# Performance work log

Measured on AMD Instinct MI355X. Metric: run time of the kernel, lower is better.

## Reference

```python
import jax, jax.numpy as jnp
import numpy as np

DECAY = 0.9
BETA_OBS = 1.0
BETA_STATE = 1.0

N_OBS = 20000
N_STATES = 1024
N_ACTIONS = 64
STATE_DIM = 256
RFD = 2048


def setup_inputs() -> dict:
    key = jax.random.key(0)
    ks = jax.random.split(key, 7)
    Q = jax.random.normal(ks[0], (STATE_DIM, N_STATES), dtype=jnp.float32) / np.sqrt(STATE_DIM).astype(np.float32)
    V = jax.random.normal(ks[1], (STATE_DIM, N_ACTIONS), dtype=jnp.float32) / np.sqrt(STATE_DIM).astype(np.float32)
    W = jax.random.normal(ks[2], (RFD, STATE_DIM), dtype=jnp.float32)
    M_re = jax.random.normal(ks[3], (RFD, N_OBS), dtype=jnp.float32)
    M_im = jax.random.normal(ks[4], (RFD, N_OBS), dtype=jnp.float32)
    obs = jax.random.uniform(ks[5], (N_OBS,), dtype=jnp.float32)
    action = jax.random.uniform(ks[6], (N_ACTIONS,), dtype=jnp.float32)
    return {"Q": Q, "V": V, "W": W, "M_re": M_re, "M_im": M_im, "obs": obs, "action": action}


def reference(Q, V, W, M_re, M_im, obs, action):
    # One fused POCML step: memory write (decayed outer product), state
    # rotation via complex random-feature phase, clean_up (state-kernel
    # softmax retrieval), and obs retrieval from memory.
    D = W.shape[0]  # random_feature_dim
    M = M_re + 1j * M_im                       # [D, n_obs] complex64
    obs_c = obs.astype(jnp.complex64)
    # get_state_from_memory
    state0 = M @ obs_c                         # [D]
    # update_memory: M *= decay; M += outer(state, obs)
    M_new = DECAY * M + jnp.outer(state0, obs_c)
    # update_state: v = V @ action; phi_v = exp(1j * W @ v); state *= phi_v
    v = V @ action                             # [state_dim]
    phi_v = jnp.exp(1j * (W @ v))              # [D] complex64
    state1 = state0 * phi_v
    # clean_up: phi_Q = exp(1j * W @ Q), weights = softmax(beta*sim(phi_Q.T, state))
    phi_Q = jnp.exp(1j * (W @ Q))              # [D, n_states]
    score = BETA_STATE * (phi_Q.T @ jnp.conj(state1)).real / D  # [n_states]
    weights = jax.nn.softmax(score)
    state2 = phi_Q @ weights.astype(jnp.complex64)              # [D]
    # get_obs_from_memory: softmax(beta_obs * sim(M.T, state))
    obs_score = BETA_OBS * (M_new.T @ jnp.conj(state2)).real / D  # [n_obs]
    return jax.nn.softmax(obs_score)
```

## Files before the change

### kernel.cpp

```cpp
#include <hip/hip_runtime.h>
#include <math.h>

#define N_OBS    20000
#define N_OBS4   5000
#define N_STATES 1024
#define N_ACT    64
#define SDIM     256
#define RFD      2048
#define DECAY    0.9f

#define OFF_S0RE   0
#define OFF_S0IM   2048
#define OFF_S1RE   4096
#define OFF_S1IM   6144
#define OFF_S2RE   8192
#define OFF_S2IM   10240
#define OFF_SCORE  12288
#define OFF_DOT0   13312
#define OFF_OBSACC 13316
#define OFF_WTS    33316
#define OFF_COSQ   34816
#define OFF_SINQ   (34816 + RFD*N_STATES)
#define WS_FLOATS  (OFF_SINQ + RFD*N_STATES)
#define ZERO_OFF   OFF_SCORE
#define ZERO_CNT   (OFF_OBSACC + N_OBS - OFF_SCORE)

__global__ __launch_bounds__(256) void k_state0(
    const float* __restrict__ Mre, const float* __restrict__ Mim,
    const float* __restrict__ obs, float* __restrict__ s0re, float* __restrict__ s0im)
{
    __shared__ float r1[256], r2[256];
    const int d = blockIdx.x, tid = threadIdx.x;
    const float4* mr = (const float4*)(Mre + (size_t)d * N_OBS);
    const float4* mi = (const float4*)(Mim + (size_t)d * N_OBS);
    const float4* ob = (const float4*)obs;
    float ar = 0.f, ai = 0.f;
    for (int idx = tid; idx < N_OBS4; idx += 256) {
        float4 o = ob[idx];
        float4 a = mr[idx];
        float4 b = mi[idx];
        ar += a.x*o.x + a.y*o.y + a.z*o.z + a.w*o.w;
        ai += b.x*o.x + b.y*o.y + b.z*o.z + b.w*o.w;
    }
    r1[tid] = ar; r2[tid] = ai; __syncthreads();
    for (int s = 128; s > 0; s >>= 1) {
        if (tid < s) { r1[tid] += r1[tid+s]; r2[tid] += r2[tid+s]; }
        __syncthreads();
    }
    if (tid == 0) { s0re[d] = r1[0]; s0im[d] = r2[0]; }
}

__global__ __launch_bounds__(256) void k_state1(
    const float* __restrict__ V, const float* __restrict__ action,
    const float* __restrict__ W,
    const float* __restrict__ s0re, const float* __restrict__ s0im,
    float* __restrict__ s1re, float* __restrict__ s1im)
{
    __shared__ float vsh[SDIM];
    const int tid = threadIdx.x;
    float acc = 0.f;
    for (int a = 0; a < N_ACT; a++) acc += V[tid * N_ACT + a] * action[a];
    vsh[tid] = acc;
    __syncthreads();
    const int d = blockIdx.x * 256 + tid;
    const float* wr = W + (size_t)d * SDIM;
    float th = 0.f;
    #pragma unroll 8
    for (int k = 0; k < SDIM; k++) th += wr[k] * vsh[k];
    float sn, cs;
    sincosf(th, &sn, &cs);
    const float re = s0re[d], im = s0im[d];
    s1re[d] = re * cs - im * sn;
    s1im[d] = re * sn + im * cs;
}

__global__ __launch_bounds__(256) void k_phiQ(
    const float* __restrict__ W, const float* __restrict__ Q,
    const float* __restrict__ s1re, const float* __restrict__ s1im,
    float* __restrict__ cosQ, float* __restrict__ sinQ, float* __restrict__ score)
{
    __shared__ float As[16][65];
    __shared__ float Bs[16][64];
    __shared__ float sscore[64];
    const int tid = threadIdx.x;
    const int tx = tid & 15;
    const int ty = tid >> 4;
    const int m0 = blockIdx.y * 64;
    const int n0 = blockIdx.x * 64;
    float c[4][4] = {};
    for (int k0 = 0; k0 < SDIM; k0 += 16) {
        {
            int k = tid & 15, mb = tid >> 4;
            #pragma unroll
            for (int j = 0; j < 4; j++)
                As[k][mb + 16*j] = W[(size_t)(m0 + mb + 16*j) * SDIM + k0 + k];
        }
        {
            int n = tid & 63, kb = tid >> 6;
            #pragma unroll
            for (int j = 0; j < 4; j++)
                Bs[kb + 4*j][n] = Q[(size_t)(k0 + kb + 4*j) * N_STATES + n0 + n];
        }
        __syncthreads();
        #pragma unroll
        for (int kk = 0; kk < 16; kk++) {
            float a[4], b[4];
            #pragma unroll
            for (int i = 0; i < 4; i++) a[i] = As[kk][ty*4 + i];
            #pragma unroll
            for (int j = 0; j < 4; j++) b[j] = Bs[kk][tx*4 + j];
            #pragma unroll
            for (int i = 0; i < 4; i++)
                #pragma unroll
                for (int j = 0; j < 4; j++)
                    c[i][j] += a[i] * b[j];
        }
        __syncthreads();
    }
    if (tid < 64) sscore[tid] = 0.f;
    __syncthreads();
    float sre[4], sim[4];
    #pragma unroll
    for (int i = 0; i < 4; i++) {
        int d = m0 + ty*4 + i;
        sre[i] = s1re[d]; sim[i] = s1im[d];
    }
    #pragma unroll
    for (int j = 0; j < 4; j++) {
        float pj = 0.f;
        #pragma unroll
        for (int i = 0; i < 4; i++) {
            int d = m0 + ty*4 + i;
            int s = n0 + tx*4 + j;
            float sn, cs;
            sincosf(c[i][j], &sn, &cs);
            cosQ[(size_t)d * N_STATES + s] = cs;
            sinQ[(size_t)d * N_STATES + s] = sn;
            pj += cs * sre[i] + sn * sim[i];
        }
        atomicAdd(&sscore[tx*4 + j], pj);
    }
    __syncthreads();
    if (tid < 64) atomicAdd(&score[n0 + tid], sscore[tid]);
}

__global__ __launch_bounds__(256) void k_softmax_w(
    const float* __restrict__ score, float* __restrict__ wts)
{
    __shared__ float red[256];
    const int tid = threadIdx.x;
    const float scale = 1.f / (float)RFD;
    float4 v = ((const float4*)score)[tid];
    v.x *= scale; v.y *= scale; v.z *= scale; v.w *= scale;
    float mx = fmaxf(fmaxf(v.x, v.y), fmaxf(v.z, v.w));
    red[tid] = mx; __syncthreads();
    for (int s = 128; s > 0; s >>= 1) {
        if (tid < s) red[tid] = fmaxf(red[tid], red[tid+s]);
        __syncthreads();
    }
    mx = red[0]; __syncthreads();
    float4 e;
    e.x = expf(v.x - mx); e.y = expf(v.y - mx);
    e.z = expf(v.z - mx); e.w = expf(v.w - mx);
    red[tid] = e.x + e.y + e.z + e.w; __syncthreads();
    for (int s = 128; s > 0; s >>= 1) {
        if (tid < s) red[tid] += red[tid+s];
        __syncthreads();
    }
    const float inv = 1.f / red[0];
    e.x *= inv; e.y *= inv; e.z *= inv; e.w *= inv;
    ((float4*)wts)[tid] = e;
}

__global__ __launch_bounds__(256) void k_state2(
    const float* __restrict__ cosQ, const float* __restrict__ sinQ,
    const float* __restrict__ wts,
    const float* __restrict__ s0re, const float* __restrict__ s0im,
    float* __restrict__ s2re, float* __restrict__ s2im, float* __restrict__ dot0)
{
    __shared__ float r1[256], r2[256];
    const int d = blockIdx.x, tid = threadIdx.x;
    float4 w = ((const float4*)wts)[tid];
    float4 a = ((const float4*)(cosQ + (size_t)d * N_STATES))[tid];
    float4 b = ((const float4*)(sinQ + (size_t)d * N_STATES))[tid];
    r1[tid] = a.x*w.x + a.y*w.y + a.z*w.z + a.w*w.w;
    r2[tid] = b.x*w.x + b.y*w.y + b.z*w.z + b.w*w.w;
    __syncthreads();
    for (int s = 128; s > 0; s >>= 1) {
        if (tid < s) { r1[tid] += r1[tid+s]; r2[tid] += r2[tid+s]; }
        __syncthreads();
    }
    if (tid == 0) {
        float rc = r1[0], rs = r2[0];
        s2re[d] = rc; s2im[d] = rs;
        atomicAdd(dot0, s0re[d]*rc + s0im[d]*rs);
    }
}

__global__ __launch_bounds__(256) void k_obs_acc(
    const float* __restrict__ Mre, const float* __restrict__ Mim,
    const float* __restrict__ s2re, const float* __restrict__ s2im,
    float* __restrict__ obs_acc)
{
    __shared__ float c_s[64], s_s[64];
    const int tid = threadIdx.x;
    const int dbase = blockIdx.y * 64;
    if (tid < 64) { c_s[tid] = s2re[dbase + tid]; s_s[tid] = s2im[dbase + tid]; }
    __syncthreads();
    const int idx = blockIdx.x * 256 + tid;
    if (idx < N_OBS4) {
        const float4* mr = (const float4*)Mre;
        const float4* mi = (const float4*)Mim;
        float4 acc = make_float4(0.f, 0.f, 0.f, 0.f);
        #pragma unroll 4
        for (int j = 0; j < 64; j++) {
            size_t base = (size_t)(dbase + j) * N_OBS4 + idx;
            float4 a = mr[base];
            float4 b = mi[base];
            float cc = c_s[j], ss = s_s[j];
            acc.x += a.x*cc + b.x*ss;
            acc.y += a.y*cc + b.y*ss;
            acc.z += a.z*cc + b.z*ss;
            acc.w += a.w*cc + b.w*ss;
        }
        atomicAdd(&obs_acc[idx*4 + 0], acc.x);
        atomicAdd(&obs_acc[idx*4 + 1], acc.y);
        atomicAdd(&obs_acc[idx*4 + 2], acc.z);
        atomicAdd(&obs_acc[idx*4 + 3], acc.w);
    }
}

__global__ __launch_bounds__(1024) void k_softmax_obs(
    const float* __restrict__ obs_acc, const float* __restrict__ obs,
    const float* __restrict__ dot0, float* __restrict__ out)
{
    __shared__ float red[1024];
    const int tid = threadIdx.x;
    const float d0 = *dot0;
    const float scale = 1.f / (float)RFD;
    float vals[20];
    float mx = -3.402823466e+38f;
    #pragma unroll
    for (int i = 0; i < 20; i++) {
        int idx = tid + i * 1024;
        if (idx < N_OBS) {
            float sc = (DECAY * obs_acc[idx] + obs[idx] * d0) * scale;
            vals[i] = sc;
            mx = fmaxf(mx, sc);
        } else vals[i] = -3.402823466e+38f;
    }
    red[tid] = mx; __syncthreads();
    for (int s = 512; s > 0; s >>= 1) {
        if (tid < s) red[tid] = fmaxf(red[tid], red[tid+s]);
        __syncthreads();
    }
    mx = red[0]; __syncthreads();
    float sum = 0.f;
    #pragma unroll
    for (int i = 0; i < 20; i++) {
        int idx = tid + i * 1024;
        if (idx < N_OBS) {
            vals[i] = expf(vals[i] - mx);
            sum += vals[i];
        }
    }
    red[tid] = sum; __syncthreads();
    for (int s = 512; s > 0; s >>= 1) {
        if (tid < s) red[tid] += red[tid+s];
        __syncthreads();
    }
    const float inv = 1.f / red[0];
    #pragma unroll
    for (int i = 0; i < 20; i++) {
        int idx = tid + i * 1024;
        if (idx < N_OBS) out[idx] = vals[i] * inv;
    }
}

extern "C" void kernel_launch(void* const* d_in, const int* in_sizes, int n_in,
                              void* d_out, int out_size, void* d_ws, size_t ws_size,
                              hipStream_t stream) {
    const float* Q      = (const float*)d_in[0];
    const float* V      = (const float*)d_in[1];
    const float* W      = (const float*)d_in[2];
    const float* Mre    = (const float*)d_in[3];
    const float* Mim    = (const float*)d_in[4];
    const float* obs    = (const float*)d_in[5];
    const float* action = (const float*)d_in[6];
    float* out = (float*)d_out;
    float* ws  = (float*)d_ws;

    if (ws_size < (size_t)WS_FLOATS * sizeof(float)) return;

    float* s0re  = ws + OFF_S0RE;
    float* s0im  = ws + OFF_S0IM;
    float* s1re  = ws + OFF_S1RE;
    float* s1im  = ws + OFF_S1IM;
    float* s2re  = ws + OFF_S2RE;
    float* s2im  = ws + OFF_S2IM;
    float* score = ws + OFF_SCORE;
    float* dot0  = ws + OFF_DOT0;
    float* oacc  = ws + OFF_OBSACC;
    float* wts   = ws + OFF_WTS;
    float* cosQ  = ws + OFF_COSQ;
    float* sinQ  = ws + OFF_SINQ;

    hipMemsetAsync(ws + ZERO_OFF, 0, (size_t)ZERO_CNT * sizeof(float), stream);

    k_state0<<<RFD, 256, 0, stream>>>(Mre, Mim, obs, s0re, s0im);
    k_state1<<<RFD / 256, 256, 0, stream>>>(V, action, W, s0re, s0im, s1re, s1im);
    k_phiQ<<<dim3(N_STATES / 64, RFD / 64), 256, 0, stream>>>(W, Q, s1re, s1im, cosQ, sinQ, score);
    k_softmax_w<<<1, 256, 0, stream>>>(score, wts);
    k_state2<<<RFD, 256, 0, stream>>>(cosQ, sinQ, wts, s0re, s0im, s2re, s2im, dot0);
    k_obs_acc<<<dim3((N_OBS4 + 255) / 256, RFD / 64), 256, 0, stream>>>(Mre, Mim, s2re, s2im, oacc);
    k_softmax_obs<<<1, 1024, 0, stream>>>(oacc, obs, dot0, out);
}
```

Baseline: 489.0 us.

## Split state0 reduction across segments and halve obs_acc row chunk

```diff
diff --git a/kernel.cpp b/kernel.cpp
--- a/kernel.cpp
+++ b/kernel.cpp
@@ -11,43 +11,53 @@
 
 #define OFF_S0RE   0
 #define OFF_S0IM   2048
-#define OFF_S1RE   4096
-#define OFF_S1IM   6144
-#define OFF_S2RE   8192
-#define OFF_S2IM   10240
-#define OFF_SCORE  12288
-#define OFF_DOT0   13312
-#define OFF_OBSACC 13316
-#define OFF_WTS    33316
+#define OFF_SCORE  4096
+#define OFF_OBSACC 5120
+#define ZERO_CNT   (OFF_OBSACC + N_OBS)
+#define OFF_S1RE   25120
+#define OFF_S1IM   27168
+#define OFF_S2RE   29216
+#define OFF_S2IM   31264
+#define OFF_WTS    33312
 #define OFF_COSQ   34816
 #define OFF_SINQ   (34816 + RFD*N_STATES)
 #define WS_FLOATS  (OFF_SINQ + RFD*N_STATES)
-#define ZERO_OFF   OFF_SCORE
-#define ZERO_CNT   (OFF_OBSACC + N_OBS - OFF_SCORE)
 
 __global__ __launch_bounds__(256) void k_state0(
     const float* __restrict__ Mre, const float* __restrict__ Mim,
     const float* __restrict__ obs, float* __restrict__ s0re, float* __restrict__ s0im)
 {
-    __shared__ float r1[256], r2[256];
-    const int d = blockIdx.x, tid = threadIdx.x;
-    const float4* mr = (const float4*)(Mre + (size_t)d * N_OBS);
-    const float4* mi = (const float4*)(Mim + (size_t)d * N_OBS);
-    const float4* ob = (const float4*)obs;
+    const int d = blockIdx.y;
+    const int seg = blockIdx.x;
+    const int tid = threadIdx.x;
+    const float4* mr = (const float4*)(Mre + (size_t)d * N_OBS) + seg * 500;
+    const float4* mi = (const float4*)(Mim + (size_t)d * N_OBS) + seg * 500;
+    const float4* ob = (const float4*)obs + seg * 500;
     float ar = 0.f, ai = 0.f;
-    for (int idx = tid; idx < N_OBS4; idx += 256) {
-        float4 o = ob[idx];
-        float4 a = mr[idx];
-        float4 b = mi[idx];
-        ar += a.x*o.x + a.y*o.y + a.z*o.z + a.w*o.w;
-        ai += b.x*o.x + b.y*o.y + b.z*o.z + b.w*o.w;
-    }
-    r1[tid] = ar; r2[tid] = ai; __syncthreads();
-    for (int s = 128; s > 0; s >>= 1) {
-        if (tid < s) { r1[tid] += r1[tid+s]; r2[tid] += r2[tid+s]; }
-        __syncthreads();
-    }
-    if (tid == 0) { s0re[d] = r1[0]; s0im[d] = r2[0]; }
+    #pragma unroll
+    for (int it = 0; it < 2; ++it) {
+        int i = tid + it * 256;
+        if (i < 500) {
+            float4 o = ob[i];
+            float4 a = mr[i];
+            float4 b = mi[i];
+            ar += a.x*o.x + a.y*o.y + a.z*o.z + a.w*o.w;
+            ai += b.x*o.x + b.y*o.y + b.z*o.z + b.w*o.w;
+        }
+    }
+    #pragma unroll
+    for (int off = 32; off > 0; off >>= 1) {
+        ar += __shfl_down(ar, off);
+        ai += __shfl_down(ai, off);
+    }
+    __shared__ float pr[4], pi[4];
+    const int wave = tid >> 6, lane = tid & 63;
+    if (lane == 0) { pr[wave] = ar; pi[wave] = ai; }
+    __syncthreads();
+    if (tid == 0) {
+        atomicAdd(&s0re[d], pr[0] + pr[1] + pr[2] + pr[3]);
+        atomicAdd(&s0im[d], pi[0] + pi[1] + pi[2] + pi[3]);
+    }
 }
 
 __global__ __launch_bounds__(256) void k_state1(
@@ -175,8 +185,7 @@
 __global__ __launch_bounds__(256) void k_state2(
     const float* __restrict__ cosQ, const float* __restrict__ sinQ,
     const float* __restrict__ wts,
-    const float* __restrict__ s0re, const float* __restrict__ s0im,
-    float* __restrict__ s2re, float* __restrict__ s2im, float* __restrict__ dot0)
+    float* __restrict__ s2re, float* __restrict__ s2im)
 {
     __shared__ float r1[256], r2[256];
     const int d = blockIdx.x, tid = threadIdx.x;
@@ -190,11 +199,7 @@
         if (tid < s) { r1[tid] += r1[tid+s]; r2[tid] += r2[tid+s]; }
         __syncthreads();
     }
-    if (tid == 0) {
-        float rc = r1[0], rs = r2[0];
-        s2re[d] = rc; s2im[d] = rs;
-        atomicAdd(dot0, s0re[d]*rc + s0im[d]*rs);
-    }
+    if (tid == 0) { s2re[d] = r1[0]; s2im[d] = r2[0]; }
 }
 
 __global__ __launch_bounds__(256) void k_obs_acc(
@@ -202,18 +207,18 @@
     const float* __restrict__ s2re, const float* __restrict__ s2im,
     float* __restrict__ obs_acc)
 {
-    __shared__ float c_s[64], s_s[64];
-    const int tid = threadIdx.x;
-    const int dbase = blockIdx.y * 64;
-    if (tid < 64) { c_s[tid] = s2re[dbase + tid]; s_s[tid] = s2im[dbase + tid]; }
+    __shared__ float c_s[32], s_s[32];
+    const int tid = threadIdx.x;
+    const int dbase = blockIdx.y * 32;
+    if (tid < 32) { c_s[tid] = s2re[dbase + tid]; s_s[tid] = s2im[dbase + tid]; }
     __syncthreads();
     const int idx = blockIdx.x * 256 + tid;
     if (idx < N_OBS4) {
         const float4* mr = (const float4*)Mre;
         const float4* mi = (const float4*)Mim;
         float4 acc = make_float4(0.f, 0.f, 0.f, 0.f);
-        #pragma unroll 4
-        for (int j = 0; j < 64; j++) {
+        #pragma unroll 8
+        for (int j = 0; j < 32; j++) {
             size_t base = (size_t)(dbase + j) * N_OBS4 + idx;
             float4 a = mr[base];
             float4 b = mi[base];
@@ -232,11 +237,25 @@
 
 __global__ __launch_bounds__(1024) void k_softmax_obs(
     const float* __restrict__ obs_acc, const float* __restrict__ obs,
-    const float* __restrict__ dot0, float* __restrict__ out)
+    const float* __restrict__ s0re, const float* __restrict__ s0im,
+    const float* __restrict__ s2re, const float* __restrict__ s2im,
+    float* __restrict__ out)
 {
     __shared__ float red[1024];
     const int tid = threadIdx.x;
-    const float d0 = *dot0;
+    float dp = 0.f;
+    #pragma unroll
+    for (int i = 0; i < 2; i++) {
+        int d = tid + i * 1024;
+        dp += s0re[d] * s2re[d] + s0im[d] * s2im[d];
+    }
+    red[tid] = dp; __syncthreads();
+    for (int s = 512; s > 0; s >>= 1) {
+        if (tid < s) red[tid] += red[tid+s];
+        __syncthreads();
+    }
+    const float d0 = red[0];
+    __syncthreads();
     const float scale = 1.f / (float)RFD;
     float vals[20];
     float mx = -3.402823466e+38f;
@@ -294,24 +313,23 @@
 
     float* s0re  = ws + OFF_S0RE;
     float* s0im  = ws + OFF_S0IM;
+    float* score = ws + OFF_SCORE;
+    float* oacc  = ws + OFF_OBSACC;
     float* s1re  = ws + OFF_S1RE;
     float* s1im  = ws + OFF_S1IM;
     float* s2re  = ws + OFF_S2RE;
     float* s2im  = ws + OFF_S2IM;
-    float* score = ws + OFF_SCORE;
-    float* dot0  = ws + OFF_DOT0;
-    float* oacc  = ws + OFF_OBSACC;
     float* wts   = ws + OFF_WTS;
     float* cosQ  = ws + OFF_COSQ;
     float* sinQ  = ws + OFF_SINQ;
 
-    hipMemsetAsync(ws + ZERO_OFF, 0, (size_t)ZERO_CNT * sizeof(float), stream);
-
-    k_state0<<<RFD, 256, 0, stream>>>(Mre, Mim, obs, s0re, s0im);
+    hipMemsetAsync(ws, 0, (size_t)ZERO_CNT * sizeof(float), stream);
+
+    k_state0<<<dim3(10, RFD), 256, 0, stream>>>(Mre, Mim, obs, s0re, s0im);
     k_state1<<<RFD / 256, 256, 0, stream>>>(V, action, W, s0re, s0im, s1re, s1im);
     k_phiQ<<<dim3(N_STATES / 64, RFD / 64), 256, 0, stream>>>(W, Q, s1re, s1im, cosQ, sinQ, score);
     k_softmax_w<<<1, 256, 0, stream>>>(score, wts);
-    k_state2<<<RFD, 256, 0, stream>>>(cosQ, sinQ, wts, s0re, s0im, s2re, s2im, dot0);
-    k_obs_acc<<<dim3((N_OBS4 + 255) / 256, RFD / 64), 256, 0, stream>>>(Mre, Mim, s2re, s2im, oacc);
-    k_softmax_obs<<<1, 1024, 0, stream>>>(oacc, obs, dot0, out);
-}
+    k_state2<<<RFD, 256, 0, stream>>>(cosQ, sinQ, wts, s2re, s2im);
+    k_obs_acc<<<dim3((N_OBS4 + 255) / 256, RFD / 32), 256, 0, stream>>>(Mre, Mim, s2re, s2im, oacc);
+    k_softmax_obs<<<1, 1024, 0, stream>>>(oacc, obs, s0re, s0im, s2re, s2im, out);
+}
```

After: 469.6 us. 1.04x faster.
